# Kernel tuning notes

Hardware: AMD Instinct MI355X
Metric: run time of the kernel (lower is better)

Reference implementation:

```python
import jax, jax.numpy as jnp
import numpy as np

B, N, D = 16, 2048, 128
SCALE = 1.0 / np.sqrt(D).astype(np.float32)


def setup_inputs() -> dict:
    key = jax.random.key(0)
    ks = jax.random.split(key, 9)
    Q = jax.random.normal(ks[0], (B, N, D), dtype=jnp.float32)
    K = jax.random.normal(ks[1], (B, N, D), dtype=jnp.float32)
    V = jax.random.normal(ks[2], (B, N, D), dtype=jnp.float32)
    bias_dis = 0.1 * jax.random.normal(ks[3], (N, N), dtype=jnp.float32)
    bias_dtw = 0.1 * jax.random.normal(ks[4], (N, N), dtype=jnp.float32)
    bias_pattern = 0.1 * jax.random.normal(ks[5], (N, N), dtype=jnp.float32)
    bias_poi = 0.1 * jax.random.normal(ks[6], (N, N), dtype=jnp.float32)
    # key/query padding masks: mostly True (valid) with some padding
    input_mask = jax.random.randint(ks[7], (B, N), 0, 10) > 0
    embeddings_mask = jax.random.randint(ks[8], (B, N), 0, 10) > 0
    # lower-triangular causal mask (diagonal kept so every row has a valid key)
    causal_mask = jnp.tril(jnp.ones((N, N), dtype=bool))
    return {"Q": Q, "K": K, "V": V, "bias_dis": bias_dis, "bias_dtw": bias_dtw,
            "bias_pattern": bias_pattern, "bias_poi": bias_poi,
            "input_mask": input_mask, "embeddings_mask": embeddings_mask,
            "causal_mask": causal_mask}


def reference(Q, K, V, bias_dis, bias_dtw, bias_pattern, bias_poi,
              input_mask, embeddings_mask, causal_mask):
    # masked_fill_(~mask, 0.0) on K, V with input_mask[:, :, None]
    km = input_mask[:, :, None]
    K = jnp.where(km, K, 0.0)
    V = jnp.where(km, V, 0.0)
    # masked_fill_(~mask, 0.0) on Q with embeddings_mask[:, :, None]
    Q = jnp.where(embeddings_mask[:, :, None], Q, 0.0)
    # scores [B, N, N] = Q K^T / sqrt(dim)
    scores = jnp.einsum('bnd,bmd->bnm', Q, K) * SCALE
    # causal masked_fill_(~causal_mask, -inf)
    scores = jnp.where(causal_mask[None, :, :], scores, -jnp.inf)
    # per-batch bias loop == broadcast add of summed [N, N] biases
    scores = scores + (bias_dis + bias_dtw + bias_pattern + bias_poi)[None, :, :]
    P = jax.nn.softmax(scores, axis=-1)
    # dropout p=0 (eval) -> identity
    return jnp.einsum('bnm,bmd->bnd', P, V)
```

## Files before the change

kernel.cpp:

```cpp
#include <hip/hip_runtime.h>
#include <math.h>

constexpr int Bc = 16;
constexpr int Nc = 2048;
constexpr int Dc = 128;
constexpr int NCHUNK = Nc / 64;
constexpr float SCALE_F = 0.08838834764831845f;

typedef __bf16 bf16x8 __attribute__((ext_vector_type(8)));
typedef __bf16 bf16x4 __attribute__((ext_vector_type(4)));
typedef float  f32x4  __attribute__((ext_vector_type(4)));

constexpr size_t KPACK_BYTES = (size_t)Bc * NCHUNK * 16 * 64 * 16;
constexpr size_t VPACK_BYTES = KPACK_BYTES;
constexpr size_t BIAS_BYTES  = (size_t)Nc * Nc * 4;
constexpr int CHUNK_ELEMS = 16 * 64 * 8;

__device__ __forceinline__ void gload_lds16(const __bf16* gsrc, __bf16* ldst) {
    __builtin_amdgcn_global_load_lds(
        (const __attribute__((address_space(1))) unsigned int*)gsrc,
        (__attribute__((address_space(3))) unsigned int*)ldst, 16, 0, 0);
}

template<int CTRL>
__device__ __forceinline__ float dpp_mv(float v) {
    return __builtin_bit_cast(float,
        __builtin_amdgcn_update_dpp(0, __builtin_bit_cast(int, v),
                                    CTRL, 0xF, 0xF, true));
}
__device__ __forceinline__ float rmax16(float v) {
    v = fmaxf(v, dpp_mv<0xB1>(v));
    v = fmaxf(v, dpp_mv<0x4E>(v));
    v = fmaxf(v, dpp_mv<0x141>(v));
    v = fmaxf(v, dpp_mv<0x140>(v));
    return v;
}
__device__ __forceinline__ float rsum16(float v) {
    v += dpp_mv<0xB1>(v);
    v += dpp_mv<0x4E>(v);
    v += dpp_mv<0x141>(v);
    v += dpp_mv<0x140>(v);
    return v;
}

__global__ __launch_bounds__(256) void prep_fused(
    const float* __restrict__ K, const float* __restrict__ V,
    const int* __restrict__ imask,
    const float* __restrict__ b0, const float* __restrict__ b1,
    const float* __restrict__ b2, const float* __restrict__ b3,
    __bf16* __restrict__ Kp, __bf16* __restrict__ Vp, float* __restrict__ bs)
{
    __shared__ __align__(16) __bf16 Ks[64][136];
    __shared__ __align__(16) __bf16 Vs[64][136];
    const int bid = blockIdx.x;
    const int tid = threadIdx.x;

    if (bid >= 512) {
        const int i = (bid - 512) * 256 + tid;
        const float4 a = ((const float4*)b0)[i];
        const float4 c = ((const float4*)b1)[i];
        const float4 d = ((const float4*)b2)[i];
        const float4 e = ((const float4*)b3)[i];
        float4 r;
        r.x = a.x + c.x + d.x + e.x;
        r.y = a.y + c.y + d.y + e.y;
        r.z = a.z + c.z + d.z + e.z;
        r.w = a.w + c.w + d.w + e.w;
        ((float4*)bs)[i] = r;
        return;
    }

    const int c = bid & 31;
    const int b = bid >> 5;
    const int m0 = c * 64;
    const float* Kb = K + (size_t)b * Nc * Dc;
    const float* Vb = V + (size_t)b * Nc * Dc;
    const int* imb = imask + b * Nc;

    #pragma unroll
    for (int it = 0; it < 8; ++it) {
        const int idx = it * 256 + tid;
        const int row = idx >> 5;
        const int c4  = idx & 31;
        const int gm  = m0 + row;
        const float msk = imb[gm] ? 1.0f : 0.0f;
        const float4 kf = ((const float4*)(Kb + (size_t)gm * Dc))[c4];
        const float4 vf = ((const float4*)(Vb + (size_t)gm * Dc))[c4];
        bf16x4 kb, vb;
        kb[0] = (__bf16)(kf.x * msk); kb[1] = (__bf16)(kf.y * msk);
        kb[2] = (__bf16)(kf.z * msk); kb[3] = (__bf16)(kf.w * msk);
        vb[0] = (__bf16)(vf.x * msk); vb[1] = (__bf16)(vf.y * msk);
        vb[2] = (__bf16)(vf.z * msk); vb[3] = (__bf16)(vf.w * msk);
        *(bf16x4*)&Ks[row][c4 * 4] = kb;
        *(bf16x4*)&Vs[row][c4 * 4] = vb;
    }
    __syncthreads();

    const size_t chunk_base = (size_t)(b * NCHUNK + c) * CHUNK_ELEMS;
    #pragma unroll
    for (int i = 0; i < 4; ++i) {
        const int s = i * 256 + tid;
        const int f = s >> 6;
        const int l = s & 63;
        const int quad = (l >> 4) & 3;
        const int l15  = l & 15;
        {
            const int jt = f >> 2, kd = f & 3;
            const bf16x8 kv = *(const bf16x8*)&Ks[jt * 16 + l15][kd * 32 + quad * 8];
            *(bf16x8*)&Kp[chunk_base + (size_t)f * 512 + l * 8] = kv;
        }
        {
            const int kj = f >> 3, dt = f & 7;
            bf16x8 vv;
            #pragma unroll
            for (int j = 0; j < 8; ++j)
                vv[j] = Vs[kj * 32 + quad * 8 + j][dt * 16 + l15];
            *(bf16x8*)&Vp[chunk_base + (size_t)f * 512 + l * 8] = vv;
        }
    }
}

__global__ __launch_bounds__(256) void attn_pipe(
    const float* __restrict__ Q,
    const __bf16* __restrict__ Kp, const __bf16* __restrict__ Vp,
    const float* __restrict__ bias, const int* __restrict__ emask,
    float* __restrict__ out)
{
    __shared__ __align__(16) __bf16 Kl[2][16 * 512];
    __shared__ __align__(16) __bf16 Vl[2][16 * 512];
    __shared__ __align__(16) __bf16 Pl[4][16][72];

    const int tid  = threadIdx.x;
    const int w    = tid >> 6;
    const int lane = tid & 63;
    const int quad = lane >> 4;
    const int l15  = lane & 15;
    const int b = blockIdx.x;
    const int s = blockIdx.y;
    const int ti  = (s < 16) ? s : (47 - s);
    const int q0w = ti * 64 + w * 16;
    const int nch = ti + 1;

    const float*  Qb  = Q + (size_t)b * Nc * Dc;
    const __bf16* Kpb = Kp + (size_t)b * NCHUNK * CHUNK_ELEMS;
    const __bf16* Vpb = Vp + (size_t)b * NCHUNK * CHUNK_ELEMS;

    const float* bp[4];
    #pragma unroll
    for (int reg = 0; reg < 4; ++reg)
        bp[reg] = bias + (size_t)(q0w + quad * 4 + reg) * Nc + l15;

    bf16x8 qfrag[4];
    {
        const int row = q0w + l15;
        const float qs = emask[b * Nc + row] ? SCALE_F : 0.0f;
        const float4* qr = (const float4*)(Qb + (size_t)row * Dc);
        #pragma unroll
        for (int kd = 0; kd < 4; ++kd) {
            const float4 xx = qr[kd * 8 + quad * 2];
            const float4 yy = qr[kd * 8 + quad * 2 + 1];
            qfrag[kd][0] = (__bf16)(xx.x * qs); qfrag[kd][1] = (__bf16)(xx.y * qs);
            qfrag[kd][2] = (__bf16)(xx.z * qs); qfrag[kd][3] = (__bf16)(xx.w * qs);
            qfrag[kd][4] = (__bf16)(yy.x * qs); qfrag[kd][5] = (__bf16)(yy.y * qs);
            qfrag[kd][6] = (__bf16)(yy.z * qs); qfrag[kd][7] = (__bf16)(yy.w * qs);
        }
    }

    f32x4 oacc[8];
    #pragma unroll
    for (int dt = 0; dt < 8; ++dt) { oacc[dt][0]=0.f; oacc[dt][1]=0.f; oacc[dt][2]=0.f; oacc[dt][3]=0.f; }
    float mrun[4] = {-INFINITY, -INFINITY, -INFINITY, -INFINITY};
    float lrun[4] = {0.f, 0.f, 0.f, 0.f};

    #pragma unroll
    for (int i = 0; i < 4; ++i) {
        const int seg = w * 4 + i;
        gload_lds16(Kpb + seg * 512 + lane * 8, &Kl[0][seg * 512]);
        gload_lds16(Vpb + seg * 512 + lane * 8, &Vl[0][seg * 512]);
    }
    float bcur[4][4], bnext[4][4];
    #pragma unroll
    for (int jt = 0; jt < 4; ++jt)
        #pragma unroll
        for (int reg = 0; reg < 4; ++reg)
            bcur[jt][reg] = bp[reg][jt * 16];
    __syncthreads();

    f32x4 sc[4];
    #pragma unroll
    for (int jt = 0; jt < 4; ++jt) { sc[jt][0]=0.f; sc[jt][1]=0.f; sc[jt][2]=0.f; sc[jt][3]=0.f; }
    #pragma unroll
    for (int jt = 0; jt < 4; ++jt)
        #pragma unroll
        for (int kd = 0; kd < 4; ++kd) {
            const bf16x8 bfr = *(const bf16x8*)&Kl[0][(jt * 4 + kd) * 512 + lane * 8];
            sc[jt] = __builtin_amdgcn_mfma_f32_16x16x32_bf16(qfrag[kd], bfr, sc[jt], 0, 0, 0);
        }
    if (nch > 1) {
        #pragma unroll
        for (int i = 0; i < 4; ++i) {
            const int seg = w * 4 + i;
            gload_lds16(Kpb + CHUNK_ELEMS + seg * 512 + lane * 8, &Kl[1][seg * 512]);
            gload_lds16(Vpb + CHUNK_ELEMS + seg * 512 + lane * 8, &Vl[1][seg * 512]);
        }
        #pragma unroll
        for (int jt = 0; jt < 4; ++jt)
            #pragma unroll
            for (int reg = 0; reg < 4; ++reg)
                bnext[jt][reg] = bp[reg][64 + jt * 16];
    }

    for (int c = 0; c < nch; ++c) {
        const int cb = c & 1;

        if (c == ti) {
            const int m0 = c * 64;
            #pragma unroll
            for (int jt = 0; jt < 4; ++jt)
                #pragma unroll
                for (int reg = 0; reg < 4; ++reg) {
                    const int gr = q0w + quad * 4 + reg;
                    const int gc = m0 + jt * 16 + l15;
                    const float v = sc[jt][reg] + bcur[jt][reg];
                    sc[jt][reg] = (gc > gr) ? -INFINITY : v;
                }
        } else {
            #pragma unroll
            for (int jt = 0; jt < 4; ++jt)
                #pragma unroll
                for (int reg = 0; reg < 4; ++reg)
                    sc[jt][reg] += bcur[jt][reg];
        }

        #pragma unroll
        for (int reg = 0; reg < 4; ++reg) {
            float mx = fmaxf(fmaxf(sc[0][reg], sc[1][reg]), fmaxf(sc[2][reg], sc[3][reg]));
            mx = rmax16(mx);
            const float mn = fmaxf(mrun[reg], mx);
            const float alpha = __expf(mrun[reg] - mn);
            mrun[reg] = mn;
            lrun[reg] *= alpha;
            #pragma unroll
            for (int dt = 0; dt < 8; ++dt) oacc[dt][reg] *= alpha;
            float ls = 0.f;
            #pragma unroll
            for (int jt = 0; jt < 4; ++jt) {
                const float pv = __expf(sc[jt][reg] - mn);
                sc[jt][reg] = pv;
                ls += pv;
            }
            lrun[reg] += rsum16(ls);
        }

        #pragma unroll
        for (int jt = 0; jt < 4; ++jt)
            #pragma unroll
            for (int reg = 0; reg < 4; ++reg)
                Pl[w][quad * 4 + reg][jt * 16 + l15] = (__bf16)sc[jt][reg];

        #pragma unroll
        for (int kj = 0; kj < 2; ++kj) {
            const bf16x8 pa = *(const bf16x8*)&Pl[w][l15][kj * 32 + quad * 8];
            #pragma unroll
            for (int dt = 0; dt < 8; ++dt) {
                const bf16x8 vb = *(const bf16x8*)&Vl[cb][(kj * 8 + dt) * 512 + lane * 8];
                oacc[dt] = __builtin_amdgcn_mfma_f32_16x16x32_bf16(pa, vb, oacc[dt], 0, 0, 0);
            }
        }

        __syncthreads();

        const bool n1 = (c + 1) < nch;
        const bool n2 = (c + 2) < nch;

        if (n2) {
            const size_t off = (size_t)(c + 2) * CHUNK_ELEMS;
            #pragma unroll
            for (int i = 0; i < 4; ++i) {
                const int seg = w * 4 + i;
                gload_lds16(Kpb + off + seg * 512 + lane * 8, &Kl[cb][seg * 512]);
                gload_lds16(Vpb + off + seg * 512 + lane * 8, &Vl[cb][seg * 512]);
            }
        }

        if (n1) {
            #pragma unroll
            for (int jt = 0; jt < 4; ++jt) { sc[jt][0]=0.f; sc[jt][1]=0.f; sc[jt][2]=0.f; sc[jt][3]=0.f; }
            #pragma unroll
            for (int jt = 0; jt < 4; ++jt)
                #pragma unroll
                for (int kd = 0; kd < 4; ++kd) {
                    const bf16x8 bfr = *(const bf16x8*)&Kl[cb ^ 1][(jt * 4 + kd) * 512 + lane * 8];
                    sc[jt] = __builtin_amdgcn_mfma_f32_16x16x32_bf16(qfrag[kd], bfr, sc[jt], 0, 0, 0);
                }
            #pragma unroll
            for (int jt = 0; jt < 4; ++jt)
                #pragma unroll
                for (int reg = 0; reg < 4; ++reg)
                    bcur[jt][reg] = bnext[jt][reg];
        }
        if (n2) {
            const int m2 = (c + 2) * 64;
            #pragma unroll
            for (int jt = 0; jt < 4; ++jt)
                #pragma unroll
                for (int reg = 0; reg < 4; ++reg)
                    bnext[jt][reg] = bp[reg][m2 + jt * 16];
        }
    }

    #pragma unroll
    for (int reg = 0; reg < 4; ++reg) {
        const float inv = 1.0f / lrun[reg];
        const int gr = q0w + quad * 4 + reg;
        float* orow = out + ((size_t)b * Nc + gr) * Dc;
        #pragma unroll
        for (int dt = 0; dt < 8; ++dt)
            orow[dt * 16 + l15] = oacc[dt][reg] * inv;
    }
}

__global__ __launch_bounds__(256) void attn_mfma_legacy(
    const float* __restrict__ Q, const float* __restrict__ K, const float* __restrict__ V,
    const float* __restrict__ p0, const float* __restrict__ p1,
    const float* __restrict__ p2, const float* __restrict__ p3,
    const int* __restrict__ imask, const int* __restrict__ emask,
    float* __restrict__ out)
{
    __shared__ __align__(16) __bf16 Klds[64][136];
    __shared__ __align__(16) __bf16 Vt[128][72];
    __shared__ __align__(16) __bf16 Plds[4][16][72];
    const int tid  = threadIdx.x;
    const int w    = tid >> 6;
    const int lane = tid & 63;
    const int quad = lane >> 4;
    const int l15  = lane & 15;
    const int b = blockIdx.y;
    const int x = blockIdx.x, yy = blockIdx.y;
    const int ti = (yy < 8) ? x : (31 - x);
    const int q0 = ti * 64, q0w = q0 + w * 16;
    const float* Qb = Q + (size_t)b * Nc * Dc;
    const float* Kb = K + (size_t)b * Nc * Dc;
    const float* Vb = V + (size_t)b * Nc * Dc;
    const int* imb = imask + b * Nc;

    bf16x8 qfrag[4];
    {
        const int row = q0w + l15;
        const float qs = emask[b * Nc + row] ? SCALE_F : 0.0f;
        const float4* qr = (const float4*)(Qb + (size_t)row * Dc);
        #pragma unroll
        for (int kd = 0; kd < 4; ++kd) {
            const float4 xv = qr[kd * 8 + quad * 2];
            const float4 yv = qr[kd * 8 + quad * 2 + 1];
            qfrag[kd][0]=(__bf16)(xv.x*qs); qfrag[kd][1]=(__bf16)(xv.y*qs);
            qfrag[kd][2]=(__bf16)(xv.z*qs); qfrag[kd][3]=(__bf16)(xv.w*qs);
            qfrag[kd][4]=(__bf16)(yv.x*qs); qfrag[kd][5]=(__bf16)(yv.y*qs);
            qfrag[kd][6]=(__bf16)(yv.z*qs); qfrag[kd][7]=(__bf16)(yv.w*qs);
        }
    }
    f32x4 oacc[8];
    #pragma unroll
    for (int dt = 0; dt < 8; ++dt){oacc[dt][0]=0.f;oacc[dt][1]=0.f;oacc[dt][2]=0.f;oacc[dt][3]=0.f;}
    float mrun[4]={-INFINITY,-INFINITY,-INFINITY,-INFINITY}, lrun[4]={0.f,0.f,0.f,0.f};

    for (int m0 = 0; m0 <= q0; m0 += 64) {
        __syncthreads();
        #pragma unroll
        for (int it = 0; it < 8; ++it) {
            const int idx = it * 256 + tid;
            const int row = idx >> 5, c4 = idx & 31;
            const int gm = m0 + row;
            const float msk = imb[gm] ? 1.0f : 0.0f;
            const float4 kf = ((const float4*)(Kb + (size_t)gm * Dc))[c4];
            const float4 vf = ((const float4*)(Vb + (size_t)gm * Dc))[c4];
            bf16x4 kb;
            kb[0]=(__bf16)(kf.x*msk); kb[1]=(__bf16)(kf.y*msk);
            kb[2]=(__bf16)(kf.z*msk); kb[3]=(__bf16)(kf.w*msk);
            *(bf16x4*)&Klds[row][c4*4] = kb;
            Vt[c4*4+0][row]=(__bf16)(vf.x*msk); Vt[c4*4+1][row]=(__bf16)(vf.y*msk);
            Vt[c4*4+2][row]=(__bf16)(vf.z*msk); Vt[c4*4+3][row]=(__bf16)(vf.w*msk);
        }
        __syncthreads();
        f32x4 sc[4];
        #pragma unroll
        for (int jt = 0; jt < 4; ++jt){sc[jt][0]=0.f;sc[jt][1]=0.f;sc[jt][2]=0.f;sc[jt][3]=0.f;}
        #pragma unroll
        for (int jt = 0; jt < 4; ++jt)
            #pragma unroll
            for (int kd = 0; kd < 4; ++kd) {
                const bf16x8 bfr = *(const bf16x8*)&Klds[jt*16+l15][kd*32+quad*8];
                sc[jt] = __builtin_amdgcn_mfma_f32_16x16x32_bf16(qfrag[kd], bfr, sc[jt], 0, 0, 0);
            }
        #pragma unroll
        for (int jt = 0; jt < 4; ++jt)
            #pragma unroll
            for (int reg = 0; reg < 4; ++reg) {
                const int gr = q0w + quad*4 + reg;
                const int gc = m0 + jt*16 + l15;
                const size_t boff = (size_t)gr * Nc + gc;
                const float bsx = p0[boff] + p1[boff] + p2[boff] + p3[boff];
                const float v = sc[jt][reg] + bsx;
                sc[jt][reg] = (gc > gr) ? -INFINITY : v;
            }
        #pragma unroll
        for (int reg = 0; reg < 4; ++reg) {
            float mx = fmaxf(fmaxf(sc[0][reg], sc[1][reg]), fmaxf(sc[2][reg], sc[3][reg]));
            mx = rmax16(mx);
            const float mn = fmaxf(mrun[reg], mx);
            const float alpha = __expf(mrun[reg] - mn);
            mrun[reg] = mn; lrun[reg] *= alpha;
            #pragma unroll
            for (int dt = 0; dt < 8; ++dt) oacc[dt][reg] *= alpha;
            float ls = 0.f;
            #pragma unroll
            for (int jt = 0; jt < 4; ++jt) {
                const float pv = __expf(sc[jt][reg] - mn);
                sc[jt][reg] = pv; ls += pv;
            }
            lrun[reg] += rsum16(ls);
        }
        #pragma unroll
        for (int jt = 0; jt < 4; ++jt)
            #pragma unroll
            for (int reg = 0; reg < 4; ++reg)
                Plds[w][quad*4+reg][jt*16+l15] = (__bf16)sc[jt][reg];
        #pragma unroll
        for (int kj = 0; kj < 2; ++kj) {
            const bf16x8 pa = *(const bf16x8*)&Plds[w][l15][kj*32+quad*8];
            #pragma unroll
            for (int dt = 0; dt < 8; ++dt) {
                const bf16x8 vb = *(const bf16x8*)&Vt[dt*16+l15][kj*32+quad*8];
                oacc[dt] = __builtin_amdgcn_mfma_f32_16x16x32_bf16(pa, vb, oacc[dt], 0, 0, 0);
            }
        }
    }
    #pragma unroll
    for (int reg = 0; reg < 4; ++reg) {
        const float inv = 1.0f / lrun[reg];
        const int gr = q0w + quad*4 + reg;
        float* orow = out + ((size_t)b * Nc + gr) * Dc;
        #pragma unroll
        for (int dt = 0; dt < 8; ++dt)
            orow[dt*16+l15] = oacc[dt][reg] * inv;
    }
}

extern "C" void kernel_launch(void* const* d_in, const int* in_sizes, int n_in,
                              void* d_out, int out_size, void* d_ws, size_t ws_size,
                              hipStream_t stream) {
    const float* Q  = (const float*)d_in[0];
    const float* K  = (const float*)d_in[1];
    const float* V  = (const float*)d_in[2];
    const float* b0 = (const float*)d_in[3];
    const float* b1 = (const float*)d_in[4];
    const float* b2 = (const float*)d_in[5];
    const float* b3 = (const float*)d_in[6];
    const int* im   = (const int*)d_in[7];
    const int* em   = (const int*)d_in[8];
    float* out      = (float*)d_out;

    if (ws_size >= KPACK_BYTES + VPACK_BYTES + BIAS_BYTES) {
        __bf16* Kp = (__bf16*)d_ws;
        __bf16* Vp = (__bf16*)((char*)d_ws + KPACK_BYTES);
        float*  bs = (float*)((char*)d_ws + KPACK_BYTES + VPACK_BYTES);
        prep_fused<<<512 + (Nc * Nc / 4) / 256, 256, 0, stream>>>(
            K, V, im, b0, b1, b2, b3, Kp, Vp, bs);
        attn_pipe<<<dim3(Bc, 32), 256, 0, stream>>>(Q, Kp, Vp, bs, em, out);
    } else {
        attn_mfma_legacy<<<dim3(NCHUNK, Bc), 256, 0, stream>>>(
            Q, K, V, b0, b1, b2, b3, im, em, out);
    }
}
```

Measured before the change: 237.0 us.

## Split KV chunks across two waves per 32-row tile and merge softmax states

Replaces the 4-wave, 64-row block with LDS double-buffered K/V by a 2-wave block covering 32 query rows. The two waves interleave over the key chunks and read packed K/V fragments straight from global memory, then merge their partial softmax states through LDS at the end. It also skips the rescale when no row max grows, and uses nontemporal loads for bias and stores for output. The intent is finer-grained causal load balancing and less block-wide synchronisation. In exchange, K/V are no longer shared through LDS across waves, and there is a final merge step.

```diff
diff --git a/kernel.cpp b/kernel.cpp
--- a/kernel.cpp
+++ b/kernel.cpp
@@ -15,12 +15,6 @@
 constexpr size_t VPACK_BYTES = KPACK_BYTES;
 constexpr size_t BIAS_BYTES  = (size_t)Nc * Nc * 4;
 constexpr int CHUNK_ELEMS = 16 * 64 * 8;
-
-__device__ __forceinline__ void gload_lds16(const __bf16* gsrc, __bf16* ldst) {
-    __builtin_amdgcn_global_load_lds(
-        (const __attribute__((address_space(1))) unsigned int*)gsrc,
-        (__attribute__((address_space(3))) unsigned int*)ldst, 16, 0, 0);
-}
 
 template<int CTRL>
 __device__ __forceinline__ float dpp_mv(float v) {
@@ -120,15 +114,16 @@
     }
 }
 
-__global__ __launch_bounds__(256) void attn_pipe(
+__global__ __launch_bounds__(128, 2) void attn_wave(
     const float* __restrict__ Q,
     const __bf16* __restrict__ Kp, const __bf16* __restrict__ Vp,
     const float* __restrict__ bias, const int* __restrict__ emask,
     float* __restrict__ out)
 {
-    __shared__ __align__(16) __bf16 Kl[2][16 * 512];
-    __shared__ __align__(16) __bf16 Vl[2][16 * 512];
-    __shared__ __align__(16) __bf16 Pl[4][16][72];
+    __shared__ __align__(16) __bf16 Pl[2][32][72];
+    __shared__ __align__(16) float  Olds[128][36];
+    __shared__ float Ml[32];
+    __shared__ float Ll[32];
 
     const int tid  = threadIdx.x;
     const int w    = tid >> 6;
@@ -136,187 +131,196 @@
     const int quad = lane >> 4;
     const int l15  = lane & 15;
     const int b = blockIdx.x;
-    const int s = blockIdx.y;
-    const int ti  = (s < 16) ? s : (47 - s);
-    const int q0w = ti * 64 + w * 16;
-    const int nch = ti + 1;
-
-    const float*  Qb  = Q + (size_t)b * Nc * Dc;
+    const int y = blockIdx.y;
+    const int t = (y < 32) ? y : ((y < 48) ? (79 - y) : (111 - y));
+    const int r0 = t * 32;
+    const int C  = (t >> 1) + 1;
+
+    const float*  Qb  = Q  + (size_t)b * Nc * Dc;
     const __bf16* Kpb = Kp + (size_t)b * NCHUNK * CHUNK_ELEMS;
     const __bf16* Vpb = Vp + (size_t)b * NCHUNK * CHUNK_ELEMS;
 
-    const float* bp[4];
-    #pragma unroll
-    for (int reg = 0; reg < 4; ++reg)
-        bp[reg] = bias + (size_t)(q0w + quad * 4 + reg) * Nc + l15;
-
-    bf16x8 qfrag[4];
-    {
-        const int row = q0w + l15;
+    bf16x8 qf[2][4];
+    #pragma unroll
+    for (int h = 0; h < 2; ++h) {
+        const int row = r0 + h * 16 + l15;
         const float qs = emask[b * Nc + row] ? SCALE_F : 0.0f;
         const float4* qr = (const float4*)(Qb + (size_t)row * Dc);
         #pragma unroll
         for (int kd = 0; kd < 4; ++kd) {
             const float4 xx = qr[kd * 8 + quad * 2];
             const float4 yy = qr[kd * 8 + quad * 2 + 1];
-            qfrag[kd][0] = (__bf16)(xx.x * qs); qfrag[kd][1] = (__bf16)(xx.y * qs);
-            qfrag[kd][2] = (__bf16)(xx.z * qs); qfrag[kd][3] = (__bf16)(xx.w * qs);
-            qfrag[kd][4] = (__bf16)(yy.x * qs); qfrag[kd][5] = (__bf16)(yy.y * qs);
-            qfrag[kd][6] = (__bf16)(yy.z * qs); qfrag[kd][7] = (__bf16)(yy.w * qs);
-        }
-    }
-
-    f32x4 oacc[8];
-    #pragma unroll
-    for (int dt = 0; dt < 8; ++dt) { oacc[dt][0]=0.f; oacc[dt][1]=0.f; oacc[dt][2]=0.f; oacc[dt][3]=0.f; }
-    float mrun[4] = {-INFINITY, -INFINITY, -INFINITY, -INFINITY};
-    float lrun[4] = {0.f, 0.f, 0.f, 0.f};
-
-    #pragma unroll
-    for (int i = 0; i < 4; ++i) {
-        const int seg = w * 4 + i;
-        gload_lds16(Kpb + seg * 512 + lane * 8, &Kl[0][seg * 512]);
-        gload_lds16(Vpb + seg * 512 + lane * 8, &Vl[0][seg * 512]);
-    }
-    float bcur[4][4], bnext[4][4];
-    #pragma unroll
-    for (int jt = 0; jt < 4; ++jt)
+            qf[h][kd][0] = (__bf16)(xx.x * qs); qf[h][kd][1] = (__bf16)(xx.y * qs);
+            qf[h][kd][2] = (__bf16)(xx.z * qs); qf[h][kd][3] = (__bf16)(xx.w * qs);
+            qf[h][kd][4] = (__bf16)(yy.x * qs); qf[h][kd][5] = (__bf16)(yy.y * qs);
+            qf[h][kd][6] = (__bf16)(yy.z * qs); qf[h][kd][7] = (__bf16)(yy.w * qs);
+        }
+    }
+
+    const float* bp[2][4];
+    #pragma unroll
+    for (int h = 0; h < 2; ++h)
         #pragma unroll
         for (int reg = 0; reg < 4; ++reg)
-            bcur[jt][reg] = bp[reg][jt * 16];
+            bp[h][reg] = bias + (size_t)(r0 + h * 16 + quad * 4 + reg) * Nc + l15;
+
+    f32x4 oacc[2][8];
+    float mrun[2][4], lrun[2][4];
+    #pragma unroll
+    for (int h = 0; h < 2; ++h) {
+        #pragma unroll
+        for (int dt = 0; dt < 8; ++dt) {
+            oacc[h][dt][0] = 0.f; oacc[h][dt][1] = 0.f;
+            oacc[h][dt][2] = 0.f; oacc[h][dt][3] = 0.f;
+        }
+        #pragma unroll
+        for (int reg = 0; reg < 4; ++reg) { mrun[h][reg] = -INFINITY; lrun[h][reg] = 0.f; }
+    }
+
+    for (int c = w; c < C; c += 2) {
+        float bc[2][4][4];
+        #pragma unroll
+        for (int h = 0; h < 2; ++h)
+            #pragma unroll
+            for (int jt = 0; jt < 4; ++jt)
+                #pragma unroll
+                for (int reg = 0; reg < 4; ++reg)
+                    bc[h][jt][reg] = __builtin_nontemporal_load(bp[h][reg] + c * 64 + jt * 16);
+
+        const size_t off = (size_t)c * CHUNK_ELEMS;
+
+        f32x4 sc[2][4];
+        #pragma unroll
+        for (int h = 0; h < 2; ++h)
+            #pragma unroll
+            for (int jt = 0; jt < 4; ++jt) {
+                sc[h][jt][0] = 0.f; sc[h][jt][1] = 0.f;
+                sc[h][jt][2] = 0.f; sc[h][jt][3] = 0.f;
+            }
+        #pragma unroll
+        for (int jt = 0; jt < 4; ++jt)
+            #pragma unroll
+            for (int kd = 0; kd < 4; ++kd) {
+                const bf16x8 kf = *(const bf16x8*)&Kpb[off + (size_t)(jt * 4 + kd) * 512 + lane * 8];
+                sc[0][jt] = __builtin_amdgcn_mfma_f32_16x16x32_bf16(qf[0][kd], kf, sc[0][jt], 0, 0, 0);
+                sc[1][jt] = __builtin_amdgcn_mfma_f32_16x16x32_bf16(qf[1][kd], kf, sc[1][jt], 0, 0, 0);
+            }
+
+        if (c == C - 1) {
+            #pragma unroll
+            for (int h = 0; h < 2; ++h)
+                #pragma unroll
+                for (int jt = 0; jt < 4; ++jt)
+                    #pragma unroll
+                    for (int reg = 0; reg < 4; ++reg) {
+                        const int gr = r0 + h * 16 + quad * 4 + reg;
+                        const int gc = c * 64 + jt * 16 + l15;
+                        const float v = sc[h][jt][reg] + bc[h][jt][reg];
+                        sc[h][jt][reg] = (gc > gr) ? -INFINITY : v;
+                    }
+        } else {
+            #pragma unroll
+            for (int h = 0; h < 2; ++h)
+                #pragma unroll
+                for (int jt = 0; jt < 4; ++jt)
+                    #pragma unroll
+                    for (int reg = 0; reg < 4; ++reg)
+                        sc[h][jt][reg] += bc[h][jt][reg];
+        }
+
+        #pragma unroll
+        for (int h = 0; h < 2; ++h) {
+            float mx[4];
+            int grow = 0;
+            #pragma unroll
+            for (int reg = 0; reg < 4; ++reg) {
+                float m = fmaxf(fmaxf(sc[h][0][reg], sc[h][1][reg]),
+                                fmaxf(sc[h][2][reg], sc[h][3][reg]));
+                m = rmax16(m);
+                mx[reg] = m;
+                grow |= (m > mrun[h][reg]);
+            }
+            if (__any(grow)) {
+                #pragma unroll
+                for (int reg = 0; reg < 4; ++reg) {
+                    const float mn = fmaxf(mrun[h][reg], mx[reg]);
+                    const float alpha = __expf(mrun[h][reg] - mn);
+                    mrun[h][reg] = mn;
+                    lrun[h][reg] *= alpha;
+                    #pragma unroll
+                    for (int dt = 0; dt < 8; ++dt) oacc[h][dt][reg] *= alpha;
+                }
+            }
+            #pragma unroll
+            for (int reg = 0; reg < 4; ++reg) {
+                float ls = 0.f;
+                #pragma unroll
+                for (int jt = 0; jt < 4; ++jt) {
+                    const float pv = __expf(sc[h][jt][reg] - mrun[h][reg]);
+                    sc[h][jt][reg] = pv;
+                    ls += pv;
+                }
+                lrun[h][reg] += rsum16(ls);
+                #pragma unroll
+                for (int jt = 0; jt < 4; ++jt)
+                    Pl[w][h * 16 + quad * 4 + reg][jt * 16 + l15] = (__bf16)sc[h][jt][reg];
+            }
+        }
+
+        #pragma unroll
+        for (int kj = 0; kj < 2; ++kj) {
+            const bf16x8 pa0 = *(const bf16x8*)&Pl[w][l15][kj * 32 + quad * 8];
+            const bf16x8 pa1 = *(const bf16x8*)&Pl[w][16 + l15][kj * 32 + quad * 8];
+            #pragma unroll
+            for (int dt = 0; dt < 8; ++dt) {
+                const bf16x8 vf = *(const bf16x8*)&Vpb[off + (size_t)(kj * 8 + dt) * 512 + lane * 8];
+                oacc[0][dt] = __builtin_amdgcn_mfma_f32_16x16x32_bf16(pa0, vf, oacc[0][dt], 0, 0, 0);
+                oacc[1][dt] = __builtin_amdgcn_mfma_f32_16x16x32_bf16(pa1, vf, oacc[1][dt], 0, 0, 0);
+            }
+        }
+    }
+
+    if (w == 1) {
+        #pragma unroll
+        for (int h = 0; h < 2; ++h) {
+            #pragma unroll
+            for (int dt = 0; dt < 8; ++dt)
+                *(f32x4*)&Olds[dt * 16 + l15][h * 16 + quad * 4] = oacc[h][dt];
+            if (l15 == 0) {
+                #pragma unroll
+                for (int reg = 0; reg < 4; ++reg) {
+                    Ml[h * 16 + quad * 4 + reg] = mrun[h][reg];
+                    Ll[h * 16 + quad * 4 + reg] = lrun[h][reg];
+                }
+            }
+        }
+    }
     __syncthreads();
-
-    f32x4 sc[4];
-    #pragma unroll
-    for (int jt = 0; jt < 4; ++jt) { sc[jt][0]=0.f; sc[jt][1]=0.f; sc[jt][2]=0.f; sc[jt][3]=0.f; }
-    #pragma unroll
-    for (int jt = 0; jt < 4; ++jt)
-        #pragma unroll
-        for (int kd = 0; kd < 4; ++kd) {
-            const bf16x8 bfr = *(const bf16x8*)&Kl[0][(jt * 4 + kd) * 512 + lane * 8];
-            sc[jt] = __builtin_amdgcn_mfma_f32_16x16x32_bf16(qfrag[kd], bfr, sc[jt], 0, 0, 0);
-        }
-    if (nch > 1) {
-        #pragma unroll
-        for (int i = 0; i < 4; ++i) {
-            const int seg = w * 4 + i;
-            gload_lds16(Kpb + CHUNK_ELEMS + seg * 512 + lane * 8, &Kl[1][seg * 512]);
-            gload_lds16(Vpb + CHUNK_ELEMS + seg * 512 + lane * 8, &Vl[1][seg * 512]);
-        }
-        #pragma unroll
-        for (int jt = 0; jt < 4; ++jt)
-            #pragma unroll
-            for (int reg = 0; reg < 4; ++reg)
-                bnext[jt][reg] = bp[reg][64 + jt * 16];
-    }
-
-    for (int c = 0; c < nch; ++c) {
-        const int cb = c & 1;
-
-        if (c == ti) {
-            const int m0 = c * 64;
-            #pragma unroll
-            for (int jt = 0; jt < 4; ++jt)
+    if (w == 0) {
+        #pragma unroll
+        for (int h = 0; h < 2; ++h) {
+            float a0[4], a1[4], linv[4];
+            #pragma unroll
+            for (int reg = 0; reg < 4; ++reg) {
+                const int rr = h * 16 + quad * 4 + reg;
+                const float m1 = Ml[rr];
+                const float l1 = Ll[rr];
+                const float m  = fmaxf(mrun[h][reg], m1);
+                a0[reg] = __expf(mrun[h][reg] - m);
+                a1[reg] = __expf(m1 - m);
+                linv[reg] = 1.0f / (lrun[h][reg] * a0[reg] + l1 * a1[reg]);
+            }
+            #pragma unroll
+            for (int dt = 0; dt < 8; ++dt) {
+                const f32x4 o1 = *(const f32x4*)&Olds[dt * 16 + l15][h * 16 + quad * 4];
                 #pragma unroll
                 for (int reg = 0; reg < 4; ++reg) {
-                    const int gr = q0w + quad * 4 + reg;
-                    const int gc = m0 + jt * 16 + l15;
-                    const float v = sc[jt][reg] + bcur[jt][reg];
-                    sc[jt][reg] = (gc > gr) ? -INFINITY : v;
+                    const int gr = r0 + h * 16 + quad * 4 + reg;
+                    const float v = (oacc[h][dt][reg] * a0[reg] + o1[reg] * a1[reg]) * linv[reg];
+                    __builtin_nontemporal_store(v, out + ((size_t)b * Nc + gr) * Dc + dt * 16 + l15);
                 }
-        } else {
-            #pragma unroll
-            for (int jt = 0; jt < 4; ++jt)
-                #pragma unroll
-                for (int reg = 0; reg < 4; ++reg)
-                    sc[jt][reg] += bcur[jt][reg];
-        }
-
-        #pragma unroll
-        for (int reg = 0; reg < 4; ++reg) {
-            float mx = fmaxf(fmaxf(sc[0][reg], sc[1][reg]), fmaxf(sc[2][reg], sc[3][reg]));
-            mx = rmax16(mx);
-            const float mn = fmaxf(mrun[reg], mx);
-            const float alpha = __expf(mrun[reg] - mn);
-            mrun[reg] = mn;
-            lrun[reg] *= alpha;
-            #pragma unroll
-            for (int dt = 0; dt < 8; ++dt) oacc[dt][reg] *= alpha;
-            float ls = 0.f;
-            #pragma unroll
-            for (int jt = 0; jt < 4; ++jt) {
-                const float pv = __expf(sc[jt][reg] - mn);
-                sc[jt][reg] = pv;
-                ls += pv;
-            }
-            lrun[reg] += rsum16(ls);
-        }
-
-        #pragma unroll
-        for (int jt = 0; jt < 4; ++jt)
-            #pragma unroll
-            for (int reg = 0; reg < 4; ++reg)
-                Pl[w][quad * 4 + reg][jt * 16 + l15] = (__bf16)sc[jt][reg];
-
-        #pragma unroll
-        for (int kj = 0; kj < 2; ++kj) {
-            const bf16x8 pa = *(const bf16x8*)&Pl[w][l15][kj * 32 + quad * 8];
-            #pragma unroll
-            for (int dt = 0; dt < 8; ++dt) {
-                const bf16x8 vb = *(const bf16x8*)&Vl[cb][(kj * 8 + dt) * 512 + lane * 8];
-                oacc[dt] = __builtin_amdgcn_mfma_f32_16x16x32_bf16(pa, vb, oacc[dt], 0, 0, 0);
-            }
-        }
-
-        __syncthreads();
-
-        const bool n1 = (c + 1) < nch;
-        const bool n2 = (c + 2) < nch;
-
-        if (n2) {
-            const size_t off = (size_t)(c + 2) * CHUNK_ELEMS;
-            #pragma unroll
-            for (int i = 0; i < 4; ++i) {
-                const int seg = w * 4 + i;
-                gload_lds16(Kpb + off + seg * 512 + lane * 8, &Kl[cb][seg * 512]);
-                gload_lds16(Vpb + off + seg * 512 + lane * 8, &Vl[cb][seg * 512]);
-            }
-        }
-
-        if (n1) {
-            #pragma unroll
-            for (int jt = 0; jt < 4; ++jt) { sc[jt][0]=0.f; sc[jt][1]=0.f; sc[jt][2]=0.f; sc[jt][3]=0.f; }
-            #pragma unroll
-            for (int jt = 0; jt < 4; ++jt)
-                #pragma unroll
-                for (int kd = 0; kd < 4; ++kd) {
-                    const bf16x8 bfr = *(const bf16x8*)&Kl[cb ^ 1][(jt * 4 + kd) * 512 + lane * 8];
-                    sc[jt] = __builtin_amdgcn_mfma_f32_16x16x32_bf16(qfrag[kd], bfr, sc[jt], 0, 0, 0);
-                }
-            #pragma unroll
-            for (int jt = 0; jt < 4; ++jt)
-                #pragma unroll
-                for (int reg = 0; reg < 4; ++reg)
-                    bcur[jt][reg] = bnext[jt][reg];
-        }
-        if (n2) {
-            const int m2 = (c + 2) * 64;
-            #pragma unroll
-            for (int jt = 0; jt < 4; ++jt)
-                #pragma unroll
-                for (int reg = 0; reg < 4; ++reg)
-                    bnext[jt][reg] = bp[reg][m2 + jt * 16];
-        }
-    }
-
-    #pragma unroll
-    for (int reg = 0; reg < 4; ++reg) {
-        const float inv = 1.0f / lrun[reg];
-        const int gr = q0w + quad * 4 + reg;
-        float* orow = out + ((size_t)b * Nc + gr) * Dc;
-        #pragma unroll
-        for (int dt = 0; dt < 8; ++dt)
-            orow[dt * 16 + l15] = oacc[dt][reg] * inv;
+            }
+        }
     }
 }
 
@@ -466,7 +470,7 @@
         float*  bs = (float*)((char*)d_ws + KPACK_BYTES + VPACK_BYTES);
         prep_fused<<<512 + (Nc * Nc / 4) / 256, 256, 0, stream>>>(
             K, V, im, b0, b1, b2, b3, Kp, Vp, bs);
-        attn_pipe<<<dim3(Bc, 32), 256, 0, stream>>>(Q, Kp, Vp, bs, em, out);
+        attn_wave<<<dim3(Bc, 64), 128, 0, stream>>>(Q, Kp, Vp, bs, em, out);
     } else {
         attn_mfma_legacy<<<dim3(NCHUNK, Bc), 256, 0, stream>>>(
             Q, K, V, b0, b1, b2, b3, im, em, out);
```

Result: slower. 248.2 us (+4.7%).

## Split long causal rows across blocks with partial merge and MFMA-packed causal bias

Applied to the files above, without the earlier changes.

Precomputes the summed bias only for the lower-triangular 32x64 tiles, stored in MFMA accumulator fragment order, so the attention kernel seeds the score accumulator directly from it. Query tiles with many key chunks are split into up to four 8-chunk pieces that write unnormalized partial outputs plus max and sum, and a new merge kernel combines them with a log-sum-exp rescale. This targets the load imbalance of causal attention and the strided bias loads. It costs extra workspace, a third kernel launch and an extra round-trip of partials through global memory.

```diff
diff --git a/kernel.cpp b/kernel.cpp
--- a/kernel.cpp
+++ b/kernel.cpp
@@ -13,8 +13,16 @@
 
 constexpr size_t KPACK_BYTES = (size_t)Bc * NCHUNK * 16 * 64 * 16;
 constexpr size_t VPACK_BYTES = KPACK_BYTES;
-constexpr size_t BIAS_BYTES  = (size_t)Nc * Nc * 4;
+constexpr int NUNITS = 1056;
+constexpr size_t BIASP_BYTES = (size_t)NUNITS * 2048 * 4;
 constexpr int CHUNK_ELEMS = 16 * 64 * 8;
+constexpr int PART_FLOATS = 64 * 128 + 64 + 64;
+constexpr size_t PART_BYTES = (size_t)Bc * 72 * PART_FLOATS * 4;
+
+__device__ __forceinline__ int ftri(int t) {
+    const int m = t >> 1;
+    return (t & 1) ? (m + 1) * (m + 1) : m * (m + 1);
+}
 
 __device__ __forceinline__ void gload_lds16(const __bf16* gsrc, __bf16* ldst) {
     __builtin_amdgcn_global_load_lds(
@@ -48,25 +56,53 @@
     const int* __restrict__ imask,
     const float* __restrict__ b0, const float* __restrict__ b1,
     const float* __restrict__ b2, const float* __restrict__ b3,
-    __bf16* __restrict__ Kp, __bf16* __restrict__ Vp, float* __restrict__ bs)
+    __bf16* __restrict__ Kp, __bf16* __restrict__ Vp, float* __restrict__ bsp)
 {
     __shared__ __align__(16) __bf16 Ks[64][136];
     __shared__ __align__(16) __bf16 Vs[64][136];
+    __shared__ __align__(16) float  Ts[32][68];
     const int bid = blockIdx.x;
     const int tid = threadIdx.x;
 
     if (bid >= 512) {
-        const int i = (bid - 512) * 256 + tid;
-        const float4 a = ((const float4*)b0)[i];
-        const float4 c = ((const float4*)b1)[i];
-        const float4 d = ((const float4*)b2)[i];
-        const float4 e = ((const float4*)b3)[i];
-        float4 r;
-        r.x = a.x + c.x + d.x + e.x;
-        r.y = a.y + c.y + d.y + e.y;
-        r.z = a.z + c.z + d.z + e.z;
-        r.w = a.w + c.w + d.w + e.w;
-        ((float4*)bs)[i] = r;
+        const int u = bid - 512;
+        int t = 0;
+        while (ftri(t + 1) <= u) ++t;
+        const int c = u - ftri(t);
+
+        #pragma unroll
+        for (int i = 0; i < 2; ++i) {
+            const int v = tid + 256 * i;
+            const int row = v >> 4, c4 = v & 15;
+            const size_t g = (size_t)(t * 32 + row) * Nc + c * 64 + c4 * 4;
+            const float4 a = *(const float4*)(b0 + g);
+            const float4 d = *(const float4*)(b1 + g);
+            const float4 e = *(const float4*)(b2 + g);
+            const float4 f = *(const float4*)(b3 + g);
+            float4 s;
+            s.x = a.x + d.x + e.x + f.x;
+            s.y = a.y + d.y + e.y + f.y;
+            s.z = a.z + d.z + e.z + f.z;
+            s.w = a.w + d.w + e.w + f.w;
+            *(float4*)&Ts[row][c4 * 4] = s;
+        }
+        __syncthreads();
+
+        const int lane = tid >> 2;
+        const int quad = lane >> 4, l15 = lane & 15;
+        const int k0 = (tid & 3) * 8;
+        float* outp = bsp + (size_t)u * 2048;
+        #pragma unroll
+        for (int g2 = 0; g2 < 2; ++g2) {
+            const int k = k0 + g2 * 4;
+            const int h = (k >> 4) & 1, jt = (k >> 2) & 3;
+            float4 o;
+            o.x = Ts[h * 16 + quad * 4 + 0][jt * 16 + l15];
+            o.y = Ts[h * 16 + quad * 4 + 1][jt * 16 + l15];
+            o.z = Ts[h * 16 + quad * 4 + 2][jt * 16 + l15];
+            o.w = Ts[h * 16 + quad * 4 + 3][jt * 16 + l15];
+            ((float4*)outp)[tid * 2 + g2] = o;
+        }
         return;
     }
 
@@ -120,11 +156,12 @@
     }
 }
 
-__global__ __launch_bounds__(256) void attn_pipe(
+template<bool SPLIT>
+__global__ __launch_bounds__(256) void attn_pipe2(
     const float* __restrict__ Q,
     const __bf16* __restrict__ Kp, const __bf16* __restrict__ Vp,
-    const float* __restrict__ bias, const int* __restrict__ emask,
-    float* __restrict__ out)
+    const float* __restrict__ biasp, const int* __restrict__ emask,
+    float* __restrict__ out, float* __restrict__ part)
 {
     __shared__ __align__(16) __bf16 Kl[2][16 * 512];
     __shared__ __align__(16) __bf16 Vl[2][16 * 512];
@@ -136,19 +173,35 @@
     const int quad = lane >> 4;
     const int l15  = lane & 15;
     const int b = blockIdx.x;
-    const int s = blockIdx.y;
-    const int ti  = (s < 16) ? s : (47 - s);
-    const int q0w = ti * 64 + w * 16;
-    const int nch = ti + 1;
+
+    int t, c0, cend, pidx;
+    bool direct;
+    if (SPLIT) {
+        const int u = 79 - blockIdx.y;
+        int s;
+        if (u < 8)       { t = u;                 s = 0; }
+        else if (u < 24) { t = 8  + ((u - 8) >> 1);  s = (u - 8) & 1; }
+        else if (u < 48) { t = 16 + (u - 24) / 3;    s = (u - 24) % 3; }
+        else             { t = 24 + ((u - 48) >> 2); s = (u - 48) & 3; }
+        c0 = s * 8;
+        cend = min(t + 1, c0 + 8);
+        direct = (u < 8);
+        pidx = u - 8;
+    } else {
+        const int y = blockIdx.y;
+        t = (y < 16) ? y : (47 - y);
+        c0 = 0; cend = t + 1; direct = true; pidx = 0;
+    }
+
+    const int q0w = t * 64 + w * 16;
+    const int t32 = t * 2 + (w >> 1);
+    const int hh  = w & 1;
+    const int fb32 = ftri(t32);
 
     const float*  Qb  = Q + (size_t)b * Nc * Dc;
     const __bf16* Kpb = Kp + (size_t)b * NCHUNK * CHUNK_ELEMS;
     const __bf16* Vpb = Vp + (size_t)b * NCHUNK * CHUNK_ELEMS;
-
-    const float* bp[4];
-    #pragma unroll
-    for (int reg = 0; reg < 4; ++reg)
-        bp[reg] = bias + (size_t)(q0w + quad * 4 + reg) * Nc + l15;
+    const f32x4* bfrag = (const f32x4*)biasp + (size_t)lane * 8 + hh * 4;
 
     bf16x8 qfrag[4];
     {
@@ -172,23 +225,23 @@
     float mrun[4] = {-INFINITY, -INFINITY, -INFINITY, -INFINITY};
     float lrun[4] = {0.f, 0.f, 0.f, 0.f};
 
+    const int nch = cend - c0;
+
     #pragma unroll
     for (int i = 0; i < 4; ++i) {
         const int seg = w * 4 + i;
-        gload_lds16(Kpb + seg * 512 + lane * 8, &Kl[0][seg * 512]);
-        gload_lds16(Vpb + seg * 512 + lane * 8, &Vl[0][seg * 512]);
-    }
-    float bcur[4][4], bnext[4][4];
+        gload_lds16(Kpb + (size_t)c0 * CHUNK_ELEMS + seg * 512 + lane * 8, &Kl[0][seg * 512]);
+        gload_lds16(Vpb + (size_t)c0 * CHUNK_ELEMS + seg * 512 + lane * 8, &Vl[0][seg * 512]);
+    }
+    f32x4 binit[4];
     #pragma unroll
     for (int jt = 0; jt < 4; ++jt)
-        #pragma unroll
-        for (int reg = 0; reg < 4; ++reg)
-            bcur[jt][reg] = bp[reg][jt * 16];
+        binit[jt] = bfrag[(size_t)(fb32 + c0) * 512 + jt];
     __syncthreads();
 
     f32x4 sc[4];
     #pragma unroll
-    for (int jt = 0; jt < 4; ++jt) { sc[jt][0]=0.f; sc[jt][1]=0.f; sc[jt][2]=0.f; sc[jt][3]=0.f; }
+    for (int jt = 0; jt < 4; ++jt) sc[jt] = binit[jt];
     #pragma unroll
     for (int jt = 0; jt < 4; ++jt)
         #pragma unroll
@@ -200,20 +253,18 @@
         #pragma unroll
         for (int i = 0; i < 4; ++i) {
             const int seg = w * 4 + i;
-            gload_lds16(Kpb + CHUNK_ELEMS + seg * 512 + lane * 8, &Kl[1][seg * 512]);
-            gload_lds16(Vpb + CHUNK_ELEMS + seg * 512 + lane * 8, &Vl[1][seg * 512]);
+            gload_lds16(Kpb + (size_t)(c0 + 1) * CHUNK_ELEMS + seg * 512 + lane * 8, &Kl[1][seg * 512]);
+            gload_lds16(Vpb + (size_t)(c0 + 1) * CHUNK_ELEMS + seg * 512 + lane * 8, &Vl[1][seg * 512]);
         }
         #pragma unroll
         for (int jt = 0; jt < 4; ++jt)
-            #pragma unroll
-            for (int reg = 0; reg < 4; ++reg)
-                bnext[jt][reg] = bp[reg][64 + jt * 16];
-    }
-
-    for (int c = 0; c < nch; ++c) {
-        const int cb = c & 1;
-
-        if (c == ti) {
+            binit[jt] = bfrag[(size_t)(fb32 + c0 + 1) * 512 + jt];
+    }
+
+    for (int c = c0; c < cend; ++c) {
+        const int cb = (c - c0) & 1;
+
+        if (c == t) {
             const int m0 = c * 64;
             #pragma unroll
             for (int jt = 0; jt < 4; ++jt)
@@ -221,15 +272,8 @@
                 for (int reg = 0; reg < 4; ++reg) {
                     const int gr = q0w + quad * 4 + reg;
                     const int gc = m0 + jt * 16 + l15;
-                    const float v = sc[jt][reg] + bcur[jt][reg];
-                    sc[jt][reg] = (gc > gr) ? -INFINITY : v;
+                    if (gc > gr) sc[jt][reg] = -INFINITY;
                 }
-        } else {
-            #pragma unroll
-            for (int jt = 0; jt < 4; ++jt)
-                #pragma unroll
-                for (int reg = 0; reg < 4; ++reg)
-                    sc[jt][reg] += bcur[jt][reg];
         }
 
         #pragma unroll
@@ -270,8 +314,8 @@
 
         __syncthreads();
 
-        const bool n1 = (c + 1) < nch;
-        const bool n2 = (c + 2) < nch;
+        const bool n1 = (c + 1) < cend;
+        const bool n2 = (c + 2) < cend;
 
         if (n2) {
             const size_t off = (size_t)(c + 2) * CHUNK_ELEMS;
@@ -285,7 +329,7 @@
 
         if (n1) {
             #pragma unroll
-            for (int jt = 0; jt < 4; ++jt) { sc[jt][0]=0.f; sc[jt][1]=0.f; sc[jt][2]=0.f; sc[jt][3]=0.f; }
+            for (int jt = 0; jt < 4; ++jt) sc[jt] = binit[jt];
             #pragma unroll
             for (int jt = 0; jt < 4; ++jt)
                 #pragma unroll
@@ -293,30 +337,79 @@
                     const bf16x8 bfr = *(const bf16x8*)&Kl[cb ^ 1][(jt * 4 + kd) * 512 + lane * 8];
                     sc[jt] = __builtin_amdgcn_mfma_f32_16x16x32_bf16(qfrag[kd], bfr, sc[jt], 0, 0, 0);
                 }
+        }
+        if (n2) {
             #pragma unroll
             for (int jt = 0; jt < 4; ++jt)
-                #pragma unroll
-                for (int reg = 0; reg < 4; ++reg)
-                    bcur[jt][reg] = bnext[jt][reg];
-        }
-        if (n2) {
-            const int m2 = (c + 2) * 64;
-            #pragma unroll
-            for (int jt = 0; jt < 4; ++jt)
-                #pragma unroll
-                for (int reg = 0; reg < 4; ++reg)
-                    bnext[jt][reg] = bp[reg][m2 + jt * 16];
-        }
-    }
-
-    #pragma unroll
-    for (int reg = 0; reg < 4; ++reg) {
-        const float inv = 1.0f / lrun[reg];
-        const int gr = q0w + quad * 4 + reg;
-        float* orow = out + ((size_t)b * Nc + gr) * Dc;
-        #pragma unroll
-        for (int dt = 0; dt < 8; ++dt)
-            orow[dt * 16 + l15] = oacc[dt][reg] * inv;
+                binit[jt] = bfrag[(size_t)(fb32 + c + 2) * 512 + jt];
+        }
+    }
+
+    if (direct) {
+        #pragma unroll
+        for (int reg = 0; reg < 4; ++reg) {
+            const float inv = 1.0f / lrun[reg];
+            const int gr = q0w + quad * 4 + reg;
+            float* orow = out + ((size_t)b * Nc + gr) * Dc;
+            #pragma unroll
+            for (int dt = 0; dt < 8; ++dt)
+                orow[dt * 16 + l15] = oacc[dt][reg] * inv;
+        }
+    } else {
+        float* pb = part + (size_t)(b * 72 + pidx) * PART_FLOATS;
+        #pragma unroll
+        for (int reg = 0; reg < 4; ++reg) {
+            const int lr = w * 16 + quad * 4 + reg;
+            #pragma unroll
+            for (int dt = 0; dt < 8; ++dt)
+                pb[lr * 128 + dt * 16 + l15] = oacc[dt][reg];
+            if (l15 == 0) {
+                pb[8192 + lr] = mrun[reg];
+                pb[8256 + lr] = lrun[reg];
+            }
+        }
+    }
+}
+
+__global__ __launch_bounds__(256) void merge_parts(
+    const float* __restrict__ part, float* __restrict__ out)
+{
+    const int b = blockIdx.x;
+    const int t = 8 + blockIdx.y;
+    const int S = (t < 16) ? 2 : ((t < 24) ? 3 : 4);
+    const int pbase = (t < 16) ? 2 * (t - 8)
+                    : (t < 24) ? 16 + 3 * (t - 16)
+                               : 40 + 4 * (t - 24);
+    const int r  = threadIdx.x >> 2;
+    const int cq = threadIdx.x & 3;
+    const float* p0 = part + (size_t)(b * 72 + pbase) * PART_FLOATS;
+
+    float m[4], a[4];
+    float mstar = -INFINITY;
+    #pragma unroll
+    for (int s = 0; s < 4; ++s)
+        if (s < S) { m[s] = p0[(size_t)s * PART_FLOATS + 8192 + r]; mstar = fmaxf(mstar, m[s]); }
+    float lsum = 0.f;
+    #pragma unroll
+    for (int s = 0; s < 4; ++s)
+        if (s < S) {
+            a[s] = __expf(m[s] - mstar);
+            lsum += p0[(size_t)s * PART_FLOATS + 8256 + r] * a[s];
+        }
+    const float inv = 1.0f / lsum;
+
+    float* orow = out + ((size_t)b * Nc + t * 64 + r) * Dc + cq * 32;
+    #pragma unroll
+    for (int i = 0; i < 8; ++i) {
+        float x = 0.f, y = 0.f, z = 0.f, ww = 0.f;
+        #pragma unroll
+        for (int s = 0; s < 4; ++s)
+            if (s < S) {
+                const f32x4 v = *(const f32x4*)&p0[(size_t)s * PART_FLOATS + r * 128 + cq * 32 + i * 4];
+                x += v[0] * a[s]; y += v[1] * a[s]; z += v[2] * a[s]; ww += v[3] * a[s];
+            }
+        f32x4 o; o[0] = x * inv; o[1] = y * inv; o[2] = z * inv; o[3] = ww * inv;
+        *(f32x4*)&orow[i * 4] = o;
     }
 }
 
@@ -460,13 +553,24 @@
     const int* em   = (const int*)d_in[8];
     float* out      = (float*)d_out;
 
-    if (ws_size >= KPACK_BYTES + VPACK_BYTES + BIAS_BYTES) {
-        __bf16* Kp = (__bf16*)d_ws;
-        __bf16* Vp = (__bf16*)((char*)d_ws + KPACK_BYTES);
-        float*  bs = (float*)((char*)d_ws + KPACK_BYTES + VPACK_BYTES);
-        prep_fused<<<512 + (Nc * Nc / 4) / 256, 256, 0, stream>>>(
-            K, V, im, b0, b1, b2, b3, Kp, Vp, bs);
-        attn_pipe<<<dim3(Bc, 32), 256, 0, stream>>>(Q, Kp, Vp, bs, em, out);
+    const size_t need_full  = KPACK_BYTES + VPACK_BYTES + BIASP_BYTES;
+    const size_t need_split = need_full + PART_BYTES;
+
+    if (ws_size >= need_full) {
+        __bf16* Kp  = (__bf16*)d_ws;
+        __bf16* Vp  = (__bf16*)((char*)d_ws + KPACK_BYTES);
+        float*  bsp = (float*)((char*)d_ws + KPACK_BYTES + VPACK_BYTES);
+        float*  prt = (float*)((char*)d_ws + need_full);
+        prep_fused<<<512 + NUNITS, 256, 0, stream>>>(
+            K, V, im, b0, b1, b2, b3, Kp, Vp, bsp);
+        if (ws_size >= need_split) {
+            attn_pipe2<true><<<dim3(Bc, 80), 256, 0, stream>>>(
+                Q, Kp, Vp, bsp, em, out, prt);
+            merge_parts<<<dim3(Bc, 24), 256, 0, stream>>>(prt, out);
+        } else {
+            attn_pipe2<false><<<dim3(Bc, 32), 256, 0, stream>>>(
+                Q, Kp, Vp, bsp, em, out, nullptr);
+        }
     } else {
         attn_mfma_legacy<<<dim3(NCHUNK, Bc), 256, 0, stream>>>(
             Q, K, V, b0, b1, b2, b3, im, em, out);
```

After: 240.3 us. About the same (+1.4%).
